# Optimization experiments

Measured on AMD Instinct MI355X. Metric: run time of the kernel, lower is better.

## Reference

```python
import jax, jax.numpy as jnp
import numpy as np
from jax import lax

BZ, CAPACITY, SEQ_LEN, IN_VAR, N_EDGES = 64, 134, 288, 16, 96


def setup_inputs() -> dict:
    key = jax.random.key(0)
    ks = jax.random.split(key, 9)
    s_gcn = 1.0 / np.sqrt(SEQ_LEN)
    s_conv = 1.0 / np.sqrt(IN_VAR * 3)
    s_fc = 1.0 / np.sqrt(2 * IN_VAR)
    return {
        "src": jax.random.normal(ks[0], (BZ, CAPACITY, SEQ_LEN, IN_VAR), dtype=jnp.float32),
        "feature_edge_index": jax.random.randint(ks[1], (2, N_EDGES), 0, IN_VAR, dtype=jnp.int32),
        # SAGEConv(seq_len, seq_len): out = lin_l(mean_neighbors) + lin_r(x); lin_l has bias
        "Wl": jax.random.uniform(ks[2], (SEQ_LEN, SEQ_LEN), jnp.float32, -s_gcn, s_gcn),
        "Wr": jax.random.uniform(ks[3], (SEQ_LEN, SEQ_LEN), jnp.float32, -s_gcn, s_gcn),
        "b_gcn": jax.random.uniform(ks[4], (SEQ_LEN,), jnp.float32, -s_gcn, s_gcn),
        "conv1_w": jax.random.uniform(ks[5], (IN_VAR, IN_VAR, 3), jnp.float32, -s_conv, s_conv),
        "conv2_w": jax.random.uniform(ks[6], (IN_VAR, IN_VAR, 5), jnp.float32, -s_conv, s_conv),
        "fc_w": jax.random.uniform(ks[7], (IN_VAR, 2 * IN_VAR), jnp.float32, -s_fc, s_fc),
        "fc_b": jax.random.uniform(ks[8], (IN_VAR,), jnp.float32, -s_fc, s_fc),
    }


def reference(src, feature_edge_index, Wl, Wr, b_gcn, conv1_w, conv2_w, fc_w, fc_b):
    bz, cap, S, F = src.shape  # [bz, capacity, seq_len, in_var]
    B = bz * cap
    # node features for the feature graph: [B, in_var, seq_len]
    x2 = src.transpose(0, 1, 3, 2).reshape(B, F, S)
    e_src, e_dst = feature_edge_index[0], feature_edge_index[1]
    # SAGEConv mean aggregation over shared edge_index, vectorized across B graphs
    gathered = x2[:, e_src, :]                                   # [B, E, S]
    agg = jnp.zeros_like(x2).at[:, e_dst, :].add(gathered)       # [B, F, S]
    deg = jnp.zeros((F,), x2.dtype).at[e_dst].add(1.0)
    mean = agg / jnp.maximum(deg, 1.0)[None, :, None]
    feat = (jnp.einsum('bns,ts->bnt', mean, Wl)
            + jnp.einsum('bns,ts->bnt', x2, Wr) + b_gcn)          # [B, F, S]
    fea_fea = feat.reshape(bz, cap, F, S).transpose(0, 1, 3, 2)   # [bz,cap,S,F]
    # dual temporal Conv1d branches (same padding, no bias) on [B, F, S]
    dn = ('NCH', 'OIH', 'NCH')
    c1 = lax.conv_general_dilated(x2, conv1_w, (1,), [(1, 1)], dimension_numbers=dn)
    c2 = lax.conv_general_dilated(x2, conv2_w, (2,), [(2, 2)][:1] * 1, dimension_numbers=dn) if False else lax.conv_general_dilated(x2, conv2_w, (1,), [(2, 2)], dimension_numbers=dn)
    temporal = (c1 + c2).transpose(0, 2, 1).reshape(bz, cap, S, F)
    com = jnp.concatenate([fea_fea, temporal], axis=-1)           # [bz,cap,S,2F]
    com = jnp.einsum('bcsf,of->bcso', com, fc_w) + fc_b
    # dropout is identity in eval mode
    return src + com
```

## Files before the change

kernel.cpp:

```cpp
#include <hip/hip_runtime.h>
#include <hip/hip_bf16.h>

typedef short short8 __attribute__((ext_vector_type(8)));
typedef float float4v __attribute__((ext_vector_type(4)));
typedef unsigned short ushort4v __attribute__((ext_vector_type(4)));

#define BTOT 8576
#define SEQ 288
#define NF 16
#define SPN 296
#define XTROWS 294
#define CATW 40
#define WCVW 104

#define XT_USH (XTROWS * 16)
#define XN_USH (16 * SPN)
#define PB (XT_USH + 2 * XN_USH)

__device__ __forceinline__ unsigned short f2b(float f) {
    union { float f; unsigned u; } v; v.f = f;
    unsigned r = v.u + 0x7FFF + ((v.u >> 16) & 1);
    return (unsigned short)(r >> 16);
}

__global__ void wcast_kernel(const float* __restrict__ a, const float* __restrict__ b,
                             unsigned short* __restrict__ o) {
    int i = blockIdx.x * 256 + threadIdx.x;
    o[i]         = f2b(a[i]);
    o[82944 + i] = f2b(b[i]);
}

#define LOADK(KK, A_, B_) do {                                                      \
    const int s0_ = ((KK) < 9 ? (KK) : (KK) - 9) * 32;                              \
    const int moff_ = ((KK) < 9) ? (XT_USH + XN_USH) : XT_USH;                      \
    (B_)[0] = *(const short8*)&pool[moff_ + li * SPN + s0_ + 8 * g];                \
    (B_)[1] = *(const short8*)&pool[PB + moff_ + li * SPN + s0_ + 8 * g];           \
    if (WPRE) {                                                                     \
        const unsigned short* Wp_ = ((KK) < 9) ? WblT : WbrT;                       \
        _Pragma("unroll")                                                           \
        for (int m_ = 0; m_ < 3; ++m_)                                              \
            if (m_ < nt)                                                            \
                (A_)[m_] = *(const short8*)&Wp_[(tts[m_] * 16 + li) * 288 + s0_ + 8 * g]; \
    } else {                                                                        \
        const float* Wp_ = ((KK) < 9) ? Wlf : Wrf;                                  \
        _Pragma("unroll")                                                           \
        for (int m_ = 0; m_ < 3; ++m_)                                              \
            if (m_ < nt) {                                                          \
                const float* p_ = &Wp_[(tts[m_] * 16 + li) * 288 + s0_ + 8 * g];    \
                float4 w0_ = *(const float4*)p_, w1_ = *(const float4*)(p_ + 4);    \
                short8 a_;                                                          \
                a_[0] = (short)f2b(w0_.x); a_[1] = (short)f2b(w0_.y);               \
                a_[2] = (short)f2b(w0_.z); a_[3] = (short)f2b(w0_.w);               \
                a_[4] = (short)f2b(w1_.x); a_[5] = (short)f2b(w1_.y);               \
                a_[6] = (short)f2b(w1_.z); a_[7] = (short)f2b(w1_.w);               \
                (A_)[m_] = a_;                                                      \
            }                                                                       \
    }                                                                               \
} while (0)

#define MFMAK(A_, B_) do {                                                          \
    _Pragma("unroll")                                                               \
    for (int m_ = 0; m_ < 3; ++m_)                                                  \
        if (m_ < nt) {                                                              \
            acc[m_][0] = __builtin_amdgcn_mfma_f32_16x16x32_bf16((A_)[m_], (B_)[0], acc[m_][0], 0, 0, 0); \
            acc[m_][1] = __builtin_amdgcn_mfma_f32_16x16x32_bf16((A_)[m_], (B_)[1], acc[m_][1], 0, 0, 0); \
        }                                                                           \
} while (0)

template<int WPRE>
__global__ __launch_bounds__(512, 4) void stconv_mfma(
    const float* __restrict__ src,
    const int*   __restrict__ eidx,
    const float* __restrict__ Wlf,
    const float* __restrict__ Wrf,
    const unsigned short* __restrict__ Wbf,
    const float* __restrict__ bgcn,
    const float* __restrict__ cw1g,
    const float* __restrict__ cw2g,
    const float* __restrict__ fcwg,
    const float* __restrict__ fcbg,
    float*       __restrict__ out)
{
    __shared__ unsigned short pool[2 * PB];
    __shared__ unsigned short wcv[16 * WCVW];
    __shared__ unsigned short fcwB[16 * 40];
    __shared__ unsigned short MB[16 * 40];
    __shared__ float bg[SEQ];
    __shared__ float Msc[256];
    __shared__ float fcb[16];

    const int tid  = threadIdx.x;
    const int wav  = tid >> 6;
    const int nb   = wav >> 2;
    const int wloc = wav & 3;
    const int lane = tid & 63;
    const int li   = lane & 15;
    const int g    = lane >> 4;
    const int b0   = blockIdx.x * 2;

    unsigned short* xsT = pool + nb * PB;
    unsigned short* xsN = pool + nb * PB + XT_USH;
    unsigned short* msN = pool + nb * PB + XT_USH + XN_USH;
    const float* srcb = src + (size_t)(b0 + nb) * (SEQ * NF);

    if (tid < 256) Msc[tid] = 0.0f;
    for (int i = tid; i < 16 * 40; i += 512) MB[i] = 0;
    for (int i = tid; i < 16 * WCVW; i += 512) wcv[i] = 0;
    if (tid < 192) {
        int nb2 = tid / 96, r2 = tid % 96;
        int r = r2 >> 4, f = r2 & 15;
        int row = (r < 2) ? r : 288 + r;
        pool[nb2 * PB + row * 16 + f] = 0;
    }
    __syncthreads();

    if (tid < 96) atomicAdd(&Msc[eidx[96 + tid] * 16 + eidx[tid]], 1.0f);
    {
        const int q = tid & 255;
        #pragma unroll
        for (int i = 0; i < 5; ++i) {
            int c = i * 256 + q;
            if (c < 1152) {
                int s = c >> 2, f0 = (c & 3) << 2;
                float4 v = *(const float4*)(srcb + (c << 2));
                ushort4v h;
                h[0] = f2b(v.x); h[1] = f2b(v.y); h[2] = f2b(v.z); h[3] = f2b(v.w);
                *(ushort4v*)&xsT[(s + 2) * 16 + f0] = h;
                xsN[(f0 + 0) * SPN + s] = h[0];
                xsN[(f0 + 1) * SPN + s] = h[1];
                xsN[(f0 + 2) * SPN + s] = h[2];
                xsN[(f0 + 3) * SPN + s] = h[3];
            }
        }
    }
    for (int j = tid; j < 1280; j += 512) {
        int fo = j / 80, rem = j % 80, fi = rem / 5, d = rem % 5;
        float t = cw2g[(fo * 16 + fi) * 5 + d];
        if (d >= 1 && d <= 3) t += cw1g[(fo * 16 + fi) * 3 + (d - 1)];
        wcv[fo * WCVW + d * 16 + fi] = f2b(t);
    }
    if (tid < 512) fcwB[(tid >> 5) * 40 + (tid & 31)] = f2b(fcwg[tid]);
    if (tid < SEQ) bg[tid] = bgcn[tid];
    if (tid < 16) fcb[tid] = fcbg[tid];
    __syncthreads();

    if (tid < 16) {
        float deg = 0.0f;
        #pragma unroll
        for (int f = 0; f < 16; ++f) deg += Msc[tid * 16 + f];
        float inv = 1.0f / fmaxf(deg, 1.0f);
        #pragma unroll
        for (int f = 0; f < 16; ++f) MB[tid * 40 + f] = f2b(Msc[tid * 16 + f] * inv);
    }
    __syncthreads();

    {
        short8 bm = *(const short8*)&MB[li * 40 + 8 * g];
        for (int st = wloc; st < 18; st += 4) {
            int s0 = st * 16;
            short8 a = {0, 0, 0, 0, 0, 0, 0, 0};
            if (g < 2) a = *(const short8*)&xsT[(s0 + li + 2) * 16 + 8 * g];
            float4v c = {0.f, 0.f, 0.f, 0.f};
            c = __builtin_amdgcn_mfma_f32_16x16x32_bf16(a, bm, c, 0, 0, 0);
            ushort4v p;
            #pragma unroll
            for (int r = 0; r < 4; ++r) p[r] = f2b(c[r]);
            *(ushort4v*)&msN[li * SPN + s0 + 4 * g] = p;
        }
    }
    __syncthreads();

    const int t2 = (wav == 0) ? 16 : ((wav == 5) ? 17 : -1);
    const int nt = (t2 >= 0) ? 3 : 2;
    const int tts[3] = {wav, wav + 8, t2};

    ushort4v p5o[3][2];
    ushort4v p6o[5];

    {
        float4v acc[3][2];
        #pragma unroll
        for (int m = 0; m < 3; ++m)
            if (m < nt) {
                #pragma unroll
                for (int r = 0; r < 4; ++r) {
                    float bv = bg[tts[m] * 16 + 4 * g + r];
                    acc[m][0][r] = bv;
                    acc[m][1][r] = bv;
                }
            }
        const unsigned short* WblT = Wbf;
        const unsigned short* WbrT = Wbf + 288 * 288;
        short8 aC[3], aN[3], bC[2], bN[2];
        LOADK(0, aC, bC);
        #pragma unroll 1
        for (int kk = 0; kk < 18; kk += 2) {
            LOADK(kk + 1, aN, bN);
            MFMAK(aC, bC);
            if (kk < 16) LOADK(kk + 2, aC, bC);
            MFMAK(aN, bN);
        }
        #pragma unroll
        for (int m = 0; m < 3; ++m)
            if (m < nt) {
                #pragma unroll
                for (int r = 0; r < 4; ++r) {
                    p5o[m][0][r] = f2b(acc[m][0][r]);
                    p5o[m][1][r] = f2b(acc[m][1][r]);
                }
            }
    }

    {
        short8 cb0 = *(const short8*)&wcv[li * WCVW + 0  + 8 * g];
        short8 cb1 = *(const short8*)&wcv[li * WCVW + 32 + 8 * g];
        short8 cb2 = *(const short8*)&wcv[li * WCVW + 64 + 8 * g];
        const int fi0   = (g & 1) * 8;
        const int dbase = g >> 1;
        #pragma unroll
        for (int it = 0; it < 5; ++it) {
            int st = wloc + 4 * it;
            if (st < 18) {
                int s0 = st * 16;
                int rbase = (s0 + li + dbase) * 16 + fi0;
                short8 a0 = *(const short8*)&xsT[rbase];
                short8 a1 = *(const short8*)&xsT[rbase + 32];
                short8 a2 = *(const short8*)&xsT[rbase + 64];
                float4v c = {0.f, 0.f, 0.f, 0.f};
                c = __builtin_amdgcn_mfma_f32_16x16x32_bf16(a0, cb0, c, 0, 0, 0);
                c = __builtin_amdgcn_mfma_f32_16x16x32_bf16(a1, cb1, c, 0, 0, 0);
                c = __builtin_amdgcn_mfma_f32_16x16x32_bf16(a2, cb2, c, 0, 0, 0);
                #pragma unroll
                for (int r = 0; r < 4; ++r) p6o[it][r] = f2b(c[r]);
            }
        }
    }
    __syncthreads();

    #pragma unroll
    for (int m = 0; m < 3; ++m)
        if (m < nt) {
            #pragma unroll
            for (int r = 0; r < 4; ++r) {
                pool[0 * PB + (tts[m] * 16 + 4 * g + r) * CATW + li] = p5o[m][0][r];
                pool[1 * PB + (tts[m] * 16 + 4 * g + r) * CATW + li] = p5o[m][1][r];
            }
        }
    #pragma unroll
    for (int it = 0; it < 5; ++it) {
        int st = wloc + 4 * it;
        if (st < 18) {
            int s0 = st * 16;
            #pragma unroll
            for (int r = 0; r < 4; ++r)
                pool[nb * PB + (s0 + 4 * g + r) * CATW + 16 + li] = p6o[it][r];
        }
    }
    __syncthreads();

    {
        const unsigned short* cat = pool + nb * PB;
        short8 fb = *(const short8*)&fcwB[li * 40 + 8 * g];
        float* outb = out + (size_t)(b0 + nb) * (SEQ * NF);
        for (int st = wloc; st < 18; st += 4) {
            int s0 = st * 16;
            float4v c;
            #pragma unroll
            for (int r = 0; r < 4; ++r) c[r] = srcb[(s0 + 4 * g + r) * 16 + li] + fcb[li];
            short8 a = *(const short8*)&cat[(s0 + li) * CATW + 8 * g];
            c = __builtin_amdgcn_mfma_f32_16x16x32_bf16(a, fb, c, 0, 0, 0);
            #pragma unroll
            for (int r = 0; r < 4; ++r) outb[(s0 + 4 * g + r) * 16 + li] = c[r];
        }
    }
}

extern "C" void kernel_launch(void* const* d_in, const int* in_sizes, int n_in,
                              void* d_out, int out_size, void* d_ws, size_t ws_size,
                              hipStream_t stream)
{
    const float* src  = (const float*)d_in[0];
    const int*   eidx = (const int*)  d_in[1];
    const float* Wl   = (const float*)d_in[2];
    const float* Wr   = (const float*)d_in[3];
    const float* bgcn = (const float*)d_in[4];
    const float* cw1  = (const float*)d_in[5];
    const float* cw2  = (const float*)d_in[6];
    const float* fcw  = (const float*)d_in[7];
    const float* fcb  = (const float*)d_in[8];
    float* out = (float*)d_out;

    const size_t wbytes = (size_t)2 * 288 * 288 * sizeof(unsigned short);
    if (ws_size >= wbytes) {
        wcast_kernel<<<dim3(324), dim3(256), 0, stream>>>(Wl, Wr, (unsigned short*)d_ws);
        stconv_mfma<1><<<dim3(BTOT / 2), dim3(512), 0, stream>>>(
            src, eidx, Wl, Wr, (const unsigned short*)d_ws,
            bgcn, cw1, cw2, fcw, fcb, out);
    } else {
        stconv_mfma<0><<<dim3(BTOT / 2), dim3(512), 0, stream>>>(
            src, eidx, Wl, Wr, nullptr,
            bgcn, cw1, cw2, fcw, fcb, out);
    }
}
```

Measured before the change: 165.3 us.

## Reassociate SAGE mean aggregation after Wl GEMM to drop msN buffer

Instead of first computing the neighbour mean (M·x) into a separate LDS buffer and then multiplying by Wl, the kernel computes x·Wr+b and x·Wl over the same xsN operand, then applies the 16x16 aggregation matrix to the Wl product with one extra MFMA. This removes the msN LDS buffer, which roughly cuts per-block shared memory by a third and allows raising launch bounds from 4 to 6 blocks per CU. The cost is an extra LDS round-trip and barrier for the G products, plus extra bf16 rounding of intermediate results (h stored as bf16 before accumulation).

Measured after the change: 232.5 us. 1.41x slower.

```diff
diff --git a/kernel.cpp b/kernel.cpp
--- a/kernel.cpp
+++ b/kernel.cpp
@@ -10,17 +10,18 @@
 #define NF 16
 #define SPN 296
 #define XTROWS 294
-#define CATW 40
-#define WCVW 104
-
 #define XT_USH (XTROWS * 16)
 #define XN_USH (16 * SPN)
-#define PB (XT_USH + 2 * XN_USH)
+#define PBN (XT_USH + XN_USH)
+#define WCVW 104
 
 __device__ __forceinline__ unsigned short f2b(float f) {
     union { float f; unsigned u; } v; v.f = f;
     unsigned r = v.u + 0x7FFF + ((v.u >> 16) & 1);
     return (unsigned short)(r >> 16);
+}
+__device__ __forceinline__ float b2f(unsigned short u) {
+    union { unsigned u; float f; } v; v.u = ((unsigned)u) << 16; return v.f;
 }
 
 __global__ void wcast_kernel(const float* __restrict__ a, const float* __restrict__ b,
@@ -30,45 +31,25 @@
     o[82944 + i] = f2b(b[i]);
 }
 
-#define LOADK(KK, A_, B_) do {                                                      \
-    const int s0_ = ((KK) < 9 ? (KK) : (KK) - 9) * 32;                              \
-    const int moff_ = ((KK) < 9) ? (XT_USH + XN_USH) : XT_USH;                      \
-    (B_)[0] = *(const short8*)&pool[moff_ + li * SPN + s0_ + 8 * g];                \
-    (B_)[1] = *(const short8*)&pool[PB + moff_ + li * SPN + s0_ + 8 * g];           \
-    if (WPRE) {                                                                     \
-        const unsigned short* Wp_ = ((KK) < 9) ? WblT : WbrT;                       \
-        _Pragma("unroll")                                                           \
-        for (int m_ = 0; m_ < 3; ++m_)                                              \
-            if (m_ < nt)                                                            \
-                (A_)[m_] = *(const short8*)&Wp_[(tts[m_] * 16 + li) * 288 + s0_ + 8 * g]; \
-    } else {                                                                        \
-        const float* Wp_ = ((KK) < 9) ? Wlf : Wrf;                                  \
-        _Pragma("unroll")                                                           \
-        for (int m_ = 0; m_ < 3; ++m_)                                              \
-            if (m_ < nt) {                                                          \
-                const float* p_ = &Wp_[(tts[m_] * 16 + li) * 288 + s0_ + 8 * g];    \
-                float4 w0_ = *(const float4*)p_, w1_ = *(const float4*)(p_ + 4);    \
-                short8 a_;                                                          \
-                a_[0] = (short)f2b(w0_.x); a_[1] = (short)f2b(w0_.y);               \
-                a_[2] = (short)f2b(w0_.z); a_[3] = (short)f2b(w0_.w);               \
-                a_[4] = (short)f2b(w1_.x); a_[5] = (short)f2b(w1_.y);               \
-                a_[6] = (short)f2b(w1_.z); a_[7] = (short)f2b(w1_.w);               \
-                (A_)[m_] = a_;                                                      \
-            }                                                                       \
-    }                                                                               \
-} while (0)
-
-#define MFMAK(A_, B_) do {                                                          \
-    _Pragma("unroll")                                                               \
-    for (int m_ = 0; m_ < 3; ++m_)                                                  \
-        if (m_ < nt) {                                                              \
-            acc[m_][0] = __builtin_amdgcn_mfma_f32_16x16x32_bf16((A_)[m_], (B_)[0], acc[m_][0], 0, 0, 0); \
-            acc[m_][1] = __builtin_amdgcn_mfma_f32_16x16x32_bf16((A_)[m_], (B_)[1], acc[m_][1], 0, 0, 0); \
-        }                                                                           \
-} while (0)
-
 template<int WPRE>
-__global__ __launch_bounds__(512, 4) void stconv_mfma(
+__device__ __forceinline__ short8 ldw(const unsigned short* __restrict__ wb,
+                                      const float* __restrict__ wf, int idx) {
+    if (WPRE) {
+        return *(const short8*)&wb[idx];
+    } else {
+        const float* p = &wf[idx];
+        float4 w0 = *(const float4*)p, w1 = *(const float4*)(p + 4);
+        short8 a;
+        a[0] = (short)f2b(w0.x); a[1] = (short)f2b(w0.y);
+        a[2] = (short)f2b(w0.z); a[3] = (short)f2b(w0.w);
+        a[4] = (short)f2b(w1.x); a[5] = (short)f2b(w1.y);
+        a[6] = (short)f2b(w1.z); a[7] = (short)f2b(w1.w);
+        return a;
+    }
+}
+
+template<int WPRE>
+__global__ __launch_bounds__(512, 6) void stconv_mfma(
     const float* __restrict__ src,
     const int*   __restrict__ eidx,
     const float* __restrict__ Wlf,
@@ -81,7 +62,7 @@
     const float* __restrict__ fcbg,
     float*       __restrict__ out)
 {
-    __shared__ unsigned short pool[2 * PB];
+    __shared__ unsigned short pool[2 * PBN];
     __shared__ unsigned short wcv[16 * WCVW];
     __shared__ unsigned short fcwB[16 * 40];
     __shared__ unsigned short MB[16 * 40];
@@ -98,9 +79,8 @@
     const int g    = lane >> 4;
     const int b0   = blockIdx.x * 2;
 
-    unsigned short* xsT = pool + nb * PB;
-    unsigned short* xsN = pool + nb * PB + XT_USH;
-    unsigned short* msN = pool + nb * PB + XT_USH + XN_USH;
+    unsigned short* xsT = pool + nb * PBN;
+    unsigned short* xsN = pool + nb * PBN + XT_USH;
     const float* srcb = src + (size_t)(b0 + nb) * (SEQ * NF);
 
     if (tid < 256) Msc[tid] = 0.0f;
@@ -110,7 +90,7 @@
         int nb2 = tid / 96, r2 = tid % 96;
         int r = r2 >> 4, f = r2 & 15;
         int row = (r < 2) ? r : 288 + r;
-        pool[nb2 * PB + row * 16 + f] = 0;
+        pool[nb2 * PBN + row * 16 + f] = 0;
     }
     __syncthreads();
 
@@ -154,63 +134,105 @@
     }
     __syncthreads();
 
-    {
-        short8 bm = *(const short8*)&MB[li * 40 + 8 * g];
-        for (int st = wloc; st < 18; st += 4) {
-            int s0 = st * 16;
-            short8 a = {0, 0, 0, 0, 0, 0, 0, 0};
-            if (g < 2) a = *(const short8*)&xsT[(s0 + li + 2) * 16 + 8 * g];
-            float4v c = {0.f, 0.f, 0.f, 0.f};
-            c = __builtin_amdgcn_mfma_f32_16x16x32_bf16(a, bm, c, 0, 0, 0);
-            ushort4v p;
-            #pragma unroll
-            for (int r = 0; r < 4; ++r) p[r] = f2b(c[r]);
-            *(ushort4v*)&msN[li * SPN + s0 + 4 * g] = p;
-        }
-    }
-    __syncthreads();
-
     const int t2 = (wav == 0) ? 16 : ((wav == 5) ? 17 : -1);
     const int nt = (t2 >= 0) ? 3 : 2;
     const int tts[3] = {wav, wav + 8, t2};
-
-    ushort4v p5o[3][2];
+    const int arow[3] = {(tts[0] * 16 + li) * 288, (tts[1] * 16 + li) * 288,
+                         (t2 >= 0) ? ((t2 * 16 + li) * 288) : 0};
+
+    const unsigned short* WblT = Wbf;
+    const unsigned short* WbrT = Wbf + 288 * 288;
+    const unsigned short* xsN0 = pool + XT_USH;
+    const unsigned short* xsN1 = pool + PBN + XT_USH;
+
+    float4v acc[3][2];
+    ushort4v hbf[3][2];
+    ushort4v gbf[3][2];
+
+    {
+        #pragma unroll
+        for (int m = 0; m < 3; ++m)
+            if (m < nt) {
+                #pragma unroll
+                for (int r = 0; r < 4; ++r) {
+                    float bv = bg[tts[m] * 16 + 4 * g + r];
+                    acc[m][0][r] = bv; acc[m][1][r] = bv;
+                }
+            }
+        short8 aC[3], aN[3];
+        #pragma unroll
+        for (int m = 0; m < 3; ++m)
+            if (m < nt) aC[m] = ldw<WPRE>(WbrT, Wrf, arow[m] + 8 * g);
+        #pragma unroll 1
+        for (int kk = 0; kk < 9; ++kk) {
+            if (kk < 8) {
+                #pragma unroll
+                for (int m = 0; m < 3; ++m)
+                    if (m < nt) aN[m] = ldw<WPRE>(WbrT, Wrf, arow[m] + (kk + 1) * 32 + 8 * g);
+            }
+            short8 bf0 = *(const short8*)&xsN0[li * SPN + kk * 32 + 8 * g];
+            short8 bf1 = *(const short8*)&xsN1[li * SPN + kk * 32 + 8 * g];
+            #pragma unroll
+            for (int m = 0; m < 3; ++m)
+                if (m < nt) {
+                    acc[m][0] = __builtin_amdgcn_mfma_f32_16x16x32_bf16(aC[m], bf0, acc[m][0], 0, 0, 0);
+                    acc[m][1] = __builtin_amdgcn_mfma_f32_16x16x32_bf16(aC[m], bf1, acc[m][1], 0, 0, 0);
+                }
+            #pragma unroll
+            for (int m = 0; m < 3; ++m) aC[m] = aN[m];
+        }
+        #pragma unroll
+        for (int m = 0; m < 3; ++m)
+            if (m < nt) {
+                #pragma unroll
+                for (int r = 0; r < 4; ++r) {
+                    hbf[m][0][r] = f2b(acc[m][0][r]);
+                    hbf[m][1][r] = f2b(acc[m][1][r]);
+                }
+            }
+    }
+
+    {
+        #pragma unroll
+        for (int m = 0; m < 3; ++m)
+            if (m < nt) {
+                #pragma unroll
+                for (int r = 0; r < 4; ++r) { acc[m][0][r] = 0.f; acc[m][1][r] = 0.f; }
+            }
+        short8 aC[3], aN[3];
+        #pragma unroll
+        for (int m = 0; m < 3; ++m)
+            if (m < nt) aC[m] = ldw<WPRE>(WblT, Wlf, arow[m] + 8 * g);
+        #pragma unroll 1
+        for (int kk = 0; kk < 9; ++kk) {
+            if (kk < 8) {
+                #pragma unroll
+                for (int m = 0; m < 3; ++m)
+                    if (m < nt) aN[m] = ldw<WPRE>(WblT, Wlf, arow[m] + (kk + 1) * 32 + 8 * g);
+            }
+            short8 bf0 = *(const short8*)&xsN0[li * SPN + kk * 32 + 8 * g];
+            short8 bf1 = *(const short8*)&xsN1[li * SPN + kk * 32 + 8 * g];
+            #pragma unroll
+            for (int m = 0; m < 3; ++m)
+                if (m < nt) {
+                    acc[m][0] = __builtin_amdgcn_mfma_f32_16x16x32_bf16(aC[m], bf0, acc[m][0], 0, 0, 0);
+                    acc[m][1] = __builtin_amdgcn_mfma_f32_16x16x32_bf16(aC[m], bf1, acc[m][1], 0, 0, 0);
+                }
+            #pragma unroll
+            for (int m = 0; m < 3; ++m) aC[m] = aN[m];
+        }
+        #pragma unroll
+        for (int m = 0; m < 3; ++m)
+            if (m < nt) {
+                #pragma unroll
+                for (int r = 0; r < 4; ++r) {
+                    gbf[m][0][r] = f2b(acc[m][0][r]);
+                    gbf[m][1][r] = f2b(acc[m][1][r]);
+                }
+            }
+    }
+
     ushort4v p6o[5];
-
-    {
-        float4v acc[3][2];
-        #pragma unroll
-        for (int m = 0; m < 3; ++m)
-            if (m < nt) {
-                #pragma unroll
-                for (int r = 0; r < 4; ++r) {
-                    float bv = bg[tts[m] * 16 + 4 * g + r];
-                    acc[m][0][r] = bv;
-                    acc[m][1][r] = bv;
-                }
-            }
-        const unsigned short* WblT = Wbf;
-        const unsigned short* WbrT = Wbf + 288 * 288;
-        short8 aC[3], aN[3], bC[2], bN[2];
-        LOADK(0, aC, bC);
-        #pragma unroll 1
-        for (int kk = 0; kk < 18; kk += 2) {
-            LOADK(kk + 1, aN, bN);
-            MFMAK(aC, bC);
-            if (kk < 16) LOADK(kk + 2, aC, bC);
-            MFMAK(aN, bN);
-        }
-        #pragma unroll
-        for (int m = 0; m < 3; ++m)
-            if (m < nt) {
-                #pragma unroll
-                for (int r = 0; r < 4; ++r) {
-                    p5o[m][0][r] = f2b(acc[m][0][r]);
-                    p5o[m][1][r] = f2b(acc[m][1][r]);
-                }
-            }
-    }
-
     {
         short8 cb0 = *(const short8*)&wcv[li * WCVW + 0  + 8 * g];
         short8 cb1 = *(const short8*)&wcv[li * WCVW + 32 + 8 * g];
@@ -237,29 +259,73 @@
     }
     __syncthreads();
 
-    #pragma unroll
-    for (int m = 0; m < 3; ++m)
-        if (m < nt) {
-            #pragma unroll
-            for (int r = 0; r < 4; ++r) {
-                pool[0 * PB + (tts[m] * 16 + 4 * g + r) * CATW + li] = p5o[m][0][r];
-                pool[1 * PB + (tts[m] * 16 + 4 * g + r) * CATW + li] = p5o[m][1][r];
-            }
-        }
-    #pragma unroll
-    for (int it = 0; it < 5; ++it) {
-        int st = wloc + 4 * it;
-        if (st < 18) {
-            int s0 = st * 16;
-            #pragma unroll
-            for (int r = 0; r < 4; ++r)
-                pool[nb * PB + (s0 + 4 * g + r) * CATW + 16 + li] = p6o[it][r];
-        }
-    }
-    __syncthreads();
-
-    {
-        const unsigned short* cat = pool + nb * PB;
+    {
+        unsigned short* Gs0 = pool + XT_USH;
+        unsigned short* Gs1 = pool + PBN + XT_USH;
+        #pragma unroll
+        for (int m = 0; m < 3; ++m)
+            if (m < nt) {
+                #pragma unroll
+                for (int r = 0; r < 4; ++r) {
+                    int p = (tts[m] * 16 + 4 * g + r) * 16 + li;
+                    Gs0[p] = gbf[m][0][r];
+                    Gs1[p] = gbf[m][1][r];
+                }
+            }
+    }
+    __syncthreads();
+
+    ushort4v p5o[3][2];
+    {
+        const unsigned short* Gs0 = pool + XT_USH;
+        const unsigned short* Gs1 = pool + PBN + XT_USH;
+        short8 mbB = *(const short8*)&MB[li * 40 + 8 * g];
+        #pragma unroll
+        for (int m = 0; m < 3; ++m)
+            if (m < nt) {
+                int t0 = tts[m] * 16;
+                short8 A0 = *(const short8*)&Gs0[(t0 + li) * 16 + 8 * g];
+                short8 A1 = *(const short8*)&Gs1[(t0 + li) * 16 + 8 * g];
+                float4v c0, c1;
+                #pragma unroll
+                for (int r = 0; r < 4; ++r) { c0[r] = b2f(hbf[m][0][r]); c1[r] = b2f(hbf[m][1][r]); }
+                c0 = __builtin_amdgcn_mfma_f32_16x16x32_bf16(A0, mbB, c0, 0, 0, 0);
+                c1 = __builtin_amdgcn_mfma_f32_16x16x32_bf16(A1, mbB, c1, 0, 0, 0);
+                #pragma unroll
+                for (int r = 0; r < 4; ++r) { p5o[m][0][r] = f2b(c0[r]); p5o[m][1][r] = f2b(c1[r]); }
+            }
+    }
+    __syncthreads();
+
+    {
+        unsigned short* cat0 = pool;
+        unsigned short* cat1 = pool + PBN;
+        #pragma unroll
+        for (int m = 0; m < 3; ++m)
+            if (m < nt) {
+                #pragma unroll
+                for (int r = 0; r < 4; ++r) {
+                    int pos = tts[m] * 16 + 4 * g + r;
+                    cat0[pos * 32 + li] = p5o[m][0][r];
+                    cat1[pos * 32 + li] = p5o[m][1][r];
+                }
+            }
+        unsigned short* catb = pool + nb * PBN;
+        #pragma unroll
+        for (int it = 0; it < 5; ++it) {
+            int st = wloc + 4 * it;
+            if (st < 18) {
+                int s0 = st * 16;
+                #pragma unroll
+                for (int r = 0; r < 4; ++r)
+                    catb[(s0 + 4 * g + r) * 32 + 16 + li] = p6o[it][r];
+            }
+        }
+    }
+    __syncthreads();
+
+    {
+        const unsigned short* catb = pool + nb * PBN;
         short8 fb = *(const short8*)&fcwB[li * 40 + 8 * g];
         float* outb = out + (size_t)(b0 + nb) * (SEQ * NF);
         for (int st = wloc; st < 18; st += 4) {
@@ -267,7 +333,7 @@
             float4v c;
             #pragma unroll
             for (int r = 0; r < 4; ++r) c[r] = srcb[(s0 + 4 * g + r) * 16 + li] + fcb[li];
-            short8 a = *(const short8*)&cat[(s0 + li) * CATW + 8 * g];
+            short8 a = *(const short8*)&catb[(s0 + li) * 32 + 8 * g];
             c = __builtin_amdgcn_mfma_f32_16x16x32_bf16(a, fb, c, 0, 0, 0);
             #pragma unroll
             for (int r = 0; r < 4; ++r) outb[(s0 + 4 * g + r) * 16 + li] = c[r];
```
